# Kernel optimization log

Hardware: AMD Instinct MI355X
Metric: run time of the kernel (lower is better)

## Reference

```python
import jax, jax.numpy as jnp
import numpy as np

D = 1024
H = 16
DH = D // H


def setup_inputs() -> dict:
    key = jax.random.key(0)
    ks = jax.random.split(key, 9)
    s = 1.0 / np.sqrt(D)
    return {
        "x": jax.random.normal(ks[0], (4, 2048, D), dtype=jnp.float32),
        "wq": jax.random.uniform(ks[1], (D, D), jnp.float32, -s, s),
        "bq": jax.random.uniform(ks[2], (D,), jnp.float32, -s, s),
        "wk": jax.random.uniform(ks[3], (D, D), jnp.float32, -s, s),
        "bk": jax.random.uniform(ks[4], (D,), jnp.float32, -s, s),
        "wv": jax.random.uniform(ks[5], (D, D), jnp.float32, -s, s),
        "bv": jax.random.uniform(ks[6], (D,), jnp.float32, -s, s),
        "wo": jax.random.uniform(ks[7], (D, D), jnp.float32, -s, s),
        "bo": jax.random.uniform(ks[8], (D,), jnp.float32, -s, s),
    }


def reference(x, wq, bq, wk, bk, wv, bv, wo, bo):
    B, S, _ = x.shape
    # projections + split heads: [B, S, D] -> [B, H, S, Dh]
    def split(t):
        return t.reshape(B, S, H, DH).transpose(0, 2, 1, 3)
    q = split(x @ wq + bq)
    k = split(x @ wk + bk)
    v = split(x @ wv + bv)
    scale = 1.0 / jnp.sqrt(jnp.float32(DH))
    scores = jnp.einsum("bhqd,bhkd->bhqk", q, k) * scale  # [B,H,S,S]
    att = jax.nn.softmax(scores, axis=-1)
    out = jnp.einsum("bhqk,bhkd->bhqd", att, v)  # [B,H,S,Dh]
    out = out.transpose(0, 2, 1, 3).reshape(B, S, D)
    return out @ wo + bo
```

## Files before the change

### kernel.cpp

```cpp
#include <hip/hip_runtime.h>
#include <stdint.h>

typedef float f32x4 __attribute__((ext_vector_type(4)));
typedef __bf16 bf16x8 __attribute__((ext_vector_type(8)));
typedef unsigned short ushort_t;
typedef ushort_t ushortx8 __attribute__((ext_vector_type(8)));
typedef ushort_t ushortx4 __attribute__((ext_vector_type(4)));

#define DEV static __device__ __forceinline__

DEV ushort_t f2bf(float f) {
  union { float f; uint32_t u; } v; v.f = f;
  uint32_t u = v.u;
  return (ushort_t)((u + 0x7FFFu + ((u >> 16) & 1u)) >> 16);
}

DEV uint32_t pkbf(float a, float b) {
  __bf16 x = (__bf16)a, y = (__bf16)b;
  return (uint32_t)__builtin_bit_cast(unsigned short, x) |
         ((uint32_t)__builtin_bit_cast(unsigned short, y) << 16);
}

DEV void cp16(const void* g, void* l) {
  __builtin_amdgcn_global_load_lds((const __attribute__((address_space(1))) unsigned int*)g,
                                   (__attribute__((address_space(3))) unsigned int*)l,
                                   16, 0, 0);
}

DEV f32x4 mfma16(bf16x8 a, bf16x8 b, f32x4 c) {
  return __builtin_amdgcn_mfma_f32_16x16x32_bf16(a, b, c, 0, 0, 0);
}

__global__ __launch_bounds__(256) void k_prep(
    const float* __restrict__ x, ushort_t* __restrict__ xb,
    const float* __restrict__ wq, const float* __restrict__ wk,
    const float* __restrict__ wv, const float* __restrict__ wo,
    ushort_t* __restrict__ wqkvT, ushort_t* __restrict__ woT) {
  __shared__ float tile[32][33];
  int b = blockIdx.x;
  if (b < 4096) {
    size_t idx = ((size_t)b * 256 + threadIdx.x) * 8;
    const float4* src = (const float4*)(x + idx);
    float4 a = src[0], c = src[1];
    ushortx8 o;
    o[0] = f2bf(a.x); o[1] = f2bf(a.y); o[2] = f2bf(a.z); o[3] = f2bf(a.w);
    o[4] = f2bf(c.x); o[5] = f2bf(c.y); o[6] = f2bf(c.z); o[7] = f2bf(c.w);
    *(ushortx8*)(xb + idx) = o;
  } else {
    int t = b - 4096;
    int which = t >> 10;
    const float* src = (which == 0) ? wq : (which == 1) ? wk : (which == 2) ? wv : wo;
    ushort_t* dst = (which == 0) ? wqkvT
                    : (which == 1) ? wqkvT + 1024 * 1024
                    : (which == 2) ? wqkvT + 2 * 1024 * 1024
                                   : woT;
    int tt = t & 1023;
    int c0 = (tt & 31) * 32, r0 = (tt >> 5) * 32;
    int tx = threadIdx.x & 31, ty = threadIdx.x >> 5;
#pragma unroll
    for (int i = ty; i < 32; i += 8)
      tile[i][tx] = src[(size_t)(r0 + i) * 1024 + c0 + tx];
    __syncthreads();
#pragma unroll
    for (int i = ty; i < 32; i += 8)
      dst[(size_t)(c0 + i) * 1024 + r0 + tx] = f2bf(tile[tx][i]);
  }
}

__global__ __launch_bounds__(256) void k_transpose_v(const ushort_t* __restrict__ vw,
                                                     ushort_t* __restrict__ vtw) {
  __shared__ ushort_t t[64][72];
  int tid = threadIdx.x;
  int bh = blockIdx.y, s0 = blockIdx.x * 64;
#pragma unroll
  for (int n = 0; n < 2; ++n) {
    int row = (tid >> 3) + n * 32, ch = (tid & 7) * 8;
    *(ushortx8*)&t[row][ch] =
        *(const ushortx8*)&vw[((size_t)bh * 2048 + s0 + row) * 64 + ch];
  }
  __syncthreads();
#pragma unroll
  for (int n = 0; n < 2; ++n) {
    int dh = (tid >> 3) + n * 32, sc = (tid & 7) * 8;
    ushortx8 o;
#pragma unroll
    for (int k = 0; k < 8; ++k) o[k] = t[sc + k][dh];
    *(ushortx8*)&vtw[((size_t)bh * 64 + dh) * 2048 + s0 + sc] = o;
  }
}

template <int MODE>
__global__ __launch_bounds__(256, 2) void k_gemm(
    const ushort_t* __restrict__ A, const ushort_t* __restrict__ Bt,
    const float* __restrict__ b0, const float* __restrict__ b1,
    const float* __restrict__ b2, ushort_t* __restrict__ qw,
    ushort_t* __restrict__ kw, ushort_t* __restrict__ vw,
    float* __restrict__ outf) {
  const int K = 1024;
  __shared__ ushort_t As[128 * 32];
  __shared__ ushort_t Bs[128 * 32];
  int tid = threadIdx.x;
  int w = tid >> 6, lane = tid & 63, l16 = lane & 15, lg = lane >> 4;
  int m0 = blockIdx.x * 128, n0 = blockIdx.y * 128;
  int wm = (w >> 1) * 64, wn = (w & 1) * 64;
  f32x4 acc[4][4] = {};

  const ushort_t* Ag = A + (size_t)(m0 + (tid >> 2)) * K + (tid & 3) * 8;
  const ushort_t* Bg = Bt + (size_t)(n0 + (tid >> 2)) * K + (tid & 3) * 8;

  for (int k0 = 0; k0 < K; k0 += 32) {
    cp16(Ag + k0, As + w * 512);
    cp16(Ag + k0 + 64 * K, As + 2048 + w * 512);
    cp16(Bg + k0, Bs + w * 512);
    cp16(Bg + k0 + 64 * K, Bs + 2048 + w * 512);
    __syncthreads();
    bf16x8 af[4], bfr[4];
#pragma unroll
    for (int i = 0; i < 4; ++i)
      af[i] = *(const bf16x8*)&As[(wm + i * 16 + l16) * 32 + lg * 8];
#pragma unroll
    for (int j = 0; j < 4; ++j)
      bfr[j] = *(const bf16x8*)&Bs[(wn + j * 16 + l16) * 32 + lg * 8];
#pragma unroll
    for (int i = 0; i < 4; ++i)
#pragma unroll
      for (int j = 0; j < 4; ++j)
        acc[i][j] = mfma16(af[i], bfr[j], acc[i][j]);
    __syncthreads();
  }

  if (MODE == 0) {
    const float QSCALE = 0.18033688011112042f;
    int p = m0 >> 10;
    const float* bias = (p == 0) ? b0 : (p == 1) ? b1 : b2;
    ushort_t* dst = (p == 0) ? qw : (p == 1) ? kw : vw;
    float qs = (p == 0) ? QSCALE : 1.0f;
    int cbase = m0 & 1023;
#pragma unroll
    for (int i = 0; i < 4; ++i) {
      int oc = cbase + wm + i * 16 + lg * 4;
      int h = oc >> 6, dh0 = oc & 63;
      float4 bb = *(const float4*)&bias[oc];
#pragma unroll
      for (int j = 0; j < 4; ++j) {
        int tok = n0 + wn + j * 16 + l16;
        size_t base =
            ((size_t)((tok >> 11) * 16 + h) * 2048 + (tok & 2047)) * 64 + dh0;
        ushortx4 pk;
        pk[0] = f2bf((acc[i][j][0] + bb.x) * qs);
        pk[1] = f2bf((acc[i][j][1] + bb.y) * qs);
        pk[2] = f2bf((acc[i][j][2] + bb.z) * qs);
        pk[3] = f2bf((acc[i][j][3] + bb.w) * qs);
        *(ushortx4*)&dst[base] = pk;
      }
    }
  } else {
#pragma unroll
    for (int j = 0; j < 4; ++j) {
      int col = n0 + wn + j * 16 + l16;
      float bb = b0[col];
#pragma unroll
      for (int i = 0; i < 4; ++i) {
#pragma unroll
        for (int r = 0; r < 4; ++r) {
          int row = m0 + wm + i * 16 + lg * 4 + r;
          outf[(size_t)row * 1024 + col] = acc[i][j][r] + bb;
        }
      }
    }
  }
}

__global__ __launch_bounds__(512, 4) void k_attn(
    const ushort_t* __restrict__ qg, const ushort_t* __restrict__ kg,
    const ushort_t* __restrict__ vtg, ushort_t* __restrict__ att) {
  __shared__ ushort_t Ks[128 * 64];
  __shared__ ushort_t Vs[64 * 128];
  __shared__ ushort_t Ps[8][16 * 128];
  int tid = threadIdx.x;
  int w = tid >> 6, lane = tid & 63, l16 = lane & 15, lg = lane >> 4;
  int i = blockIdx.x;
  int bh = (i & 7) * 8 + ((i >> 3) & 7);
  int q0 = (i >> 6) * 256;
  const ushort_t* qh = qg + (size_t)bh * 2048 * 64;

  const ushort_t* kstage = kg + (size_t)bh * 2048 * 64 + (size_t)(tid >> 3) * 64 +
                           (size_t)(((tid & 7) ^ ((tid >> 3) & 7)) * 8);
  const ushort_t* vstage = vtg + (size_t)bh * 64 * 2048 + (size_t)(tid >> 4) * 2048 +
                           (size_t)(((tid & 15) ^ ((tid >> 4) & 15)) * 8);

  bf16x8 qf[2][2];
#pragma unroll
  for (int st = 0; st < 2; ++st)
#pragma unroll
    for (int ks = 0; ks < 2; ++ks)
      qf[st][ks] = *(const bf16x8*)(qh + (size_t)(q0 + w * 32 + st * 16 + l16) * 64 +
                                    ks * 32 + lg * 8);

  bf16x8 vone;
#pragma unroll
  for (int t = 0; t < 8; ++t) vone[t] = (__bf16)1.0f;

  f32x4 o[2][5] = {};

  for (int kb = 0; kb < 2048; kb += 128) {
    __syncthreads();
    cp16(kstage + (size_t)kb * 64, Ks + w * 512);
    cp16(kstage + (size_t)(kb + 64) * 64, Ks + 4096 + w * 512);
    cp16(vstage + kb, Vs + w * 512);
    cp16(vstage + kb + (size_t)32 * 2048, Vs + 4096 + w * 512);
    __syncthreads();

#pragma unroll
    for (int hf = 0; hf < 2; ++hf) {
      f32x4 sc[2][4] = {};
#pragma unroll
      for (int jt = 0; jt < 4; ++jt) {
        int row = hf * 64 + jt * 16 + l16;
        bf16x8 kf0 = *(const bf16x8*)&Ks[row * 64 + ((lg) ^ (l16 & 7)) * 8];
        bf16x8 kf1 = *(const bf16x8*)&Ks[row * 64 + ((lg + 4) ^ (l16 & 7)) * 8];
        sc[0][jt] = mfma16(kf0, qf[0][0], sc[0][jt]);
        sc[0][jt] = mfma16(kf1, qf[0][1], sc[0][jt]);
        sc[1][jt] = mfma16(kf0, qf[1][0], sc[1][jt]);
        sc[1][jt] = mfma16(kf1, qf[1][1], sc[1][jt]);
      }
#pragma unroll
      for (int st = 0; st < 2; ++st)
#pragma unroll
        for (int jt = 0; jt < 4; ++jt) {
          float e0 = __builtin_amdgcn_exp2f(sc[st][jt][0]);
          float e1 = __builtin_amdgcn_exp2f(sc[st][jt][1]);
          float e2 = __builtin_amdgcn_exp2f(sc[st][jt][2]);
          float e3 = __builtin_amdgcn_exp2f(sc[st][jt][3]);
          uint32_t* dst =
              (uint32_t*)&Ps[w][l16 * 128 +
                                (((st * 8 + jt * 2 + (lg >> 1)) ^ l16) * 8) +
                                (lg & 1) * 4];
          dst[0] = pkbf(e0, e1);
          dst[1] = pkbf(e2, e3);
        }
#pragma unroll
      for (int ks = 0; ks < 2; ++ks) {
        int kk = hf * 2 + ks;
        bf16x8 pf0 =
            *(const bf16x8*)&Ps[w][l16 * 128 + (((ks * 4 + lg) ^ l16) * 8)];
        bf16x8 pf1 =
            *(const bf16x8*)&Ps[w][l16 * 128 + (((8 + ks * 4 + lg) ^ l16) * 8)];
        o[0][4] = mfma16(pf0, vone, o[0][4]);
        o[1][4] = mfma16(pf1, vone, o[1][4]);
#pragma unroll
        for (int dt = 0; dt < 4; ++dt) {
          int vrow = dt * 16 + l16;
          bf16x8 vf =
              *(const bf16x8*)&Vs[vrow * 128 + (((kk * 4 + lg) ^ l16) * 8)];
          o[0][dt] = mfma16(pf0, vf, o[0][dt]);
          o[1][dt] = mfma16(pf1, vf, o[1][dt]);
        }
      }
    }
  }

  int bi = bh >> 4, h = bh & 15;
#pragma unroll
  for (int st = 0; st < 2; ++st) {
    f32x4 inv;
#pragma unroll
    for (int r = 0; r < 4; ++r) inv[r] = __builtin_amdgcn_rcpf(o[st][4][r]);
#pragma unroll
    for (int dt = 0; dt < 4; ++dt)
#pragma unroll
      for (int r = 0; r < 4; ++r) {
        int srow = q0 + w * 32 + st * 16 + lg * 4 + r;
        int col = h * 64 + dt * 16 + l16;
        att[(size_t)(bi * 2048 + srow) * 1024 + col] = f2bf(o[st][dt][r] * inv[r]);
      }
  }
}

extern "C" void kernel_launch(void* const* d_in, const int* in_sizes, int n_in,
                              void* d_out, int out_size, void* d_ws, size_t ws_size,
                              hipStream_t stream) {
  const float* x = (const float*)d_in[0];
  const float* wq = (const float*)d_in[1];
  const float* bq = (const float*)d_in[2];
  const float* wk = (const float*)d_in[3];
  const float* bk = (const float*)d_in[4];
  const float* wv = (const float*)d_in[5];
  const float* bv = (const float*)d_in[6];
  const float* wo = (const float*)d_in[7];
  const float* bo = (const float*)d_in[8];
  float* out = (float*)d_out;

  char* ws = (char*)d_ws;
  ushort_t* xb = (ushort_t*)(ws);
  ushort_t* wqkvT = (ushort_t*)(ws + 16777216);
  ushort_t* woT = (ushort_t*)(ws + 23068672);
  ushort_t* qw = (ushort_t*)(ws + 25165824);
  ushort_t* kw = (ushort_t*)(ws + 41943040);
  ushort_t* vtw = (ushort_t*)(ws + 58720256);
  ushort_t* att = (ushort_t*)(ws + 75497472);
  ushort_t* vw = att;

  k_prep<<<dim3(8192), dim3(256), 0, stream>>>(x, xb, wq, wk, wv, wo, wqkvT, woT);

  k_gemm<0><<<dim3(24, 64), dim3(256), 0, stream>>>(
      wqkvT, xb, bq, bk, bv, qw, kw, vw, nullptr);

  k_transpose_v<<<dim3(32, 64), dim3(256), 0, stream>>>(vw, vtw);

  k_attn<<<dim3(512), dim3(512), 0, stream>>>(qw, kw, vtw, att);

  k_gemm<1><<<dim3(64, 8), dim3(256), 0, stream>>>(
      att, woT, bo, nullptr, nullptr, nullptr, nullptr, nullptr, out);
}
```

Measured before the change: 277.2 us.

## Rewrite attention kernel with 32x32 MFMA tiles and register row sums

The attention kernel moves from 16x16x32 to 32x32x16 bf16 MFMA and halves the block to 4 waves, each handling 64 query rows. The softmax denominator is now summed in registers from the exp values and reduced across lane halves, which removes the extra ones-vector MFMA. The larger tiles are meant to raise the ratio of matrix math to LDS reads and cut LDS traffic per FLOP. In exchange each thread carries more accumulator registers and the occupancy target drops to 3 blocks per CU.

```diff
diff --git a/kernel.cpp b/kernel.cpp
--- a/kernel.cpp
+++ b/kernel.cpp
@@ -2,10 +2,12 @@
 #include <stdint.h>
 
 typedef float f32x4 __attribute__((ext_vector_type(4)));
+typedef float f32x16 __attribute__((ext_vector_type(16)));
 typedef __bf16 bf16x8 __attribute__((ext_vector_type(8)));
 typedef unsigned short ushort_t;
 typedef ushort_t ushortx8 __attribute__((ext_vector_type(8)));
 typedef ushort_t ushortx4 __attribute__((ext_vector_type(4)));
+typedef uint32_t u32x2 __attribute__((ext_vector_type(2)));
 
 #define DEV static __device__ __forceinline__
 
@@ -29,6 +31,10 @@
 
 DEV f32x4 mfma16(bf16x8 a, bf16x8 b, f32x4 c) {
   return __builtin_amdgcn_mfma_f32_16x16x32_bf16(a, b, c, 0, 0, 0);
+}
+
+DEV f32x16 mfma32(bf16x8 a, bf16x8 b, f32x16 c) {
+  return __builtin_amdgcn_mfma_f32_32x32x16_bf16(a, b, c, 0, 0, 0);
 }
 
 __global__ __launch_bounds__(256) void k_prep(
@@ -171,14 +177,14 @@
   }
 }
 
-__global__ __launch_bounds__(512, 4) void k_attn(
+__global__ __launch_bounds__(256, 3) void k_attn(
     const ushort_t* __restrict__ qg, const ushort_t* __restrict__ kg,
     const ushort_t* __restrict__ vtg, ushort_t* __restrict__ att) {
   __shared__ ushort_t Ks[128 * 64];
   __shared__ ushort_t Vs[64 * 128];
-  __shared__ ushort_t Ps[8][16 * 128];
+  __shared__ ushort_t Ps[4][2][32 * 32];
   int tid = threadIdx.x;
-  int w = tid >> 6, lane = tid & 63, l16 = lane & 15, lg = lane >> 4;
+  int w = tid >> 6, lane = tid & 63, l32 = lane & 31, half = lane >> 5;
   int i = blockIdx.x;
   int bh = (i & 7) * 8 + ((i >> 3) & 7);
   int q0 = (i >> 6) * 256;
@@ -189,90 +195,92 @@
   const ushort_t* vstage = vtg + (size_t)bh * 64 * 2048 + (size_t)(tid >> 4) * 2048 +
                            (size_t)(((tid & 15) ^ ((tid >> 4) & 15)) * 8);
 
-  bf16x8 qf[2][2];
+  bf16x8 qf[2][4];
 #pragma unroll
   for (int st = 0; st < 2; ++st)
 #pragma unroll
-    for (int ks = 0; ks < 2; ++ks)
-      qf[st][ks] = *(const bf16x8*)(qh + (size_t)(q0 + w * 32 + st * 16 + l16) * 64 +
-                                    ks * 32 + lg * 8);
-
-  bf16x8 vone;
-#pragma unroll
-  for (int t = 0; t < 8; ++t) vone[t] = (__bf16)1.0f;
-
-  f32x4 o[2][5] = {};
+    for (int ks = 0; ks < 4; ++ks)
+      qf[st][ks] = *(const bf16x8*)(qh +
+                                    (size_t)(q0 + w * 64 + st * 32 + l32) * 64 +
+                                    ks * 16 + half * 8);
+
+  f32x16 o[2][2] = {};
+  float lsum[2] = {0.f, 0.f};
+  int swz = (l32 >> 1) & 3;
 
   for (int kb = 0; kb < 2048; kb += 128) {
     __syncthreads();
-    cp16(kstage + (size_t)kb * 64, Ks + w * 512);
-    cp16(kstage + (size_t)(kb + 64) * 64, Ks + 4096 + w * 512);
-    cp16(vstage + kb, Vs + w * 512);
-    cp16(vstage + kb + (size_t)32 * 2048, Vs + 4096 + w * 512);
-    __syncthreads();
-
-#pragma unroll
-    for (int hf = 0; hf < 2; ++hf) {
-      f32x4 sc[2][4] = {};
-#pragma unroll
-      for (int jt = 0; jt < 4; ++jt) {
-        int row = hf * 64 + jt * 16 + l16;
-        bf16x8 kf0 = *(const bf16x8*)&Ks[row * 64 + ((lg) ^ (l16 & 7)) * 8];
-        bf16x8 kf1 = *(const bf16x8*)&Ks[row * 64 + ((lg + 4) ^ (l16 & 7)) * 8];
-        sc[0][jt] = mfma16(kf0, qf[0][0], sc[0][jt]);
-        sc[0][jt] = mfma16(kf1, qf[0][1], sc[0][jt]);
-        sc[1][jt] = mfma16(kf0, qf[1][0], sc[1][jt]);
-        sc[1][jt] = mfma16(kf1, qf[1][1], sc[1][jt]);
-      }
-#pragma unroll
-      for (int st = 0; st < 2; ++st)
-#pragma unroll
-        for (int jt = 0; jt < 4; ++jt) {
-          float e0 = __builtin_amdgcn_exp2f(sc[st][jt][0]);
-          float e1 = __builtin_amdgcn_exp2f(sc[st][jt][1]);
-          float e2 = __builtin_amdgcn_exp2f(sc[st][jt][2]);
-          float e3 = __builtin_amdgcn_exp2f(sc[st][jt][3]);
-          uint32_t* dst =
-              (uint32_t*)&Ps[w][l16 * 128 +
-                                (((st * 8 + jt * 2 + (lg >> 1)) ^ l16) * 8) +
-                                (lg & 1) * 4];
-          dst[0] = pkbf(e0, e1);
-          dst[1] = pkbf(e2, e3);
+#pragma unroll
+    for (int j = 0; j < 4; ++j) {
+      cp16(kstage + (size_t)(kb + j * 32) * 64, Ks + (j * 32 + w * 8) * 64);
+      cp16(vstage + kb + (size_t)(j * 16) * 2048, Vs + (j * 16 + w * 4) * 128);
+    }
+    __syncthreads();
+
+#pragma unroll
+    for (int g = 0; g < 4; ++g) {
+      bf16x8 kf[4];
+#pragma unroll
+      for (int ks = 0; ks < 4; ++ks)
+        kf[ks] = *(const bf16x8*)&Ks[(g * 32 + l32) * 64 +
+                                     (((2 * ks + half) ^ (l32 & 7)) * 8)];
+#pragma unroll
+      for (int st = 0; st < 2; ++st) {
+        f32x16 sc = {};
+#pragma unroll
+        for (int ks = 0; ks < 4; ++ks) sc = mfma32(kf[ks], qf[st][ks], sc);
+        float ls = 0.f;
+#pragma unroll
+        for (int r = 0; r < 16; ++r) {
+          sc[r] = __builtin_amdgcn_exp2f(sc[r]);
+          ls += sc[r];
         }
-#pragma unroll
-      for (int ks = 0; ks < 2; ++ks) {
-        int kk = hf * 2 + ks;
-        bf16x8 pf0 =
-            *(const bf16x8*)&Ps[w][l16 * 128 + (((ks * 4 + lg) ^ l16) * 8)];
-        bf16x8 pf1 =
-            *(const bf16x8*)&Ps[w][l16 * 128 + (((8 + ks * 4 + lg) ^ l16) * 8)];
-        o[0][4] = mfma16(pf0, vone, o[0][4]);
-        o[1][4] = mfma16(pf1, vone, o[1][4]);
-#pragma unroll
-        for (int dt = 0; dt < 4; ++dt) {
-          int vrow = dt * 16 + l16;
-          bf16x8 vf =
-              *(const bf16x8*)&Vs[vrow * 128 + (((kk * 4 + lg) ^ l16) * 8)];
-          o[0][dt] = mfma16(pf0, vf, o[0][dt]);
-          o[1][dt] = mfma16(pf1, vf, o[1][dt]);
+        lsum[st] += ls;
+#pragma unroll
+        for (int q2 = 0; q2 < 4; ++q2) {
+          u32x2 pk;
+          pk[0] = pkbf(sc[q2 * 4 + 0], sc[q2 * 4 + 1]);
+          pk[1] = pkbf(sc[q2 * 4 + 2], sc[q2 * 4 + 3]);
+          *(u32x2*)&Ps[w][st][l32 * 32 + ((q2 ^ swz) * 8) + half * 4] = pk;
         }
       }
+#pragma unroll
+      for (int ks2 = 0; ks2 < 2; ++ks2) {
+        int pofs = l32 * 32 + (((2 * ks2 + half) ^ swz) * 8);
+        bf16x8 pf0 = *(const bf16x8*)&Ps[w][0][pofs];
+        bf16x8 pf1 = *(const bf16x8*)&Ps[w][1][pofs];
+#pragma unroll
+        for (int dt = 0; dt < 2; ++dt) {
+          bf16x8 vf = *(const bf16x8*)&Vs[(dt * 32 + l32) * 128 +
+                                          (((4 * g + 2 * ks2 + half) ^
+                                            (l32 & 15)) * 8)];
+          o[0][dt] = mfma32(pf0, vf, o[0][dt]);
+          o[1][dt] = mfma32(pf1, vf, o[1][dt]);
+        }
+      }
     }
   }
 
+  float* lp = (float*)&Ps[w][0][0];
+#pragma unroll
+  for (int st = 0; st < 2; ++st) {
+    float lt = lsum[st] + __shfl_xor(lsum[st], 32);
+    if (half == 0) lp[st * 32 + l32] = __builtin_amdgcn_rcpf(lt);
+  }
   int bi = bh >> 4, h = bh & 15;
 #pragma unroll
   for (int st = 0; st < 2; ++st) {
-    f32x4 inv;
-#pragma unroll
-    for (int r = 0; r < 4; ++r) inv[r] = __builtin_amdgcn_rcpf(o[st][4][r]);
-#pragma unroll
-    for (int dt = 0; dt < 4; ++dt)
-#pragma unroll
-      for (int r = 0; r < 4; ++r) {
-        int srow = q0 + w * 32 + st * 16 + lg * 4 + r;
-        int col = h * 64 + dt * 16 + l16;
-        att[(size_t)(bi * 2048 + srow) * 1024 + col] = f2bf(o[st][dt][r] * inv[r]);
+    float linv[16];
+#pragma unroll
+    for (int r = 0; r < 16; ++r)
+      linv[r] = lp[st * 32 + ((r & 3) + 8 * (r >> 2) + 4 * half)];
+#pragma unroll
+    for (int dt = 0; dt < 2; ++dt)
+#pragma unroll
+      for (int r = 0; r < 16; ++r) {
+        int tok = q0 + w * 64 + st * 32 + (r & 3) + 8 * (r >> 2) + 4 * half;
+        att[(size_t)(bi * 2048 + tok) * 1024 + h * 64 + dt * 32 + l32] =
+            f2bf(o[st][dt][r] * linv[r]);
       }
   }
 }
@@ -308,7 +316,7 @@
 
   k_transpose_v<<<dim3(32, 64), dim3(256), 0, stream>>>(vw, vtw);
 
-  k_attn<<<dim3(512), dim3(512), 0, stream>>>(qw, kw, vtw, att);
+  k_attn<<<dim3(512), dim3(256), 0, stream>>>(qw, kw, vtw, att);
 
   k_gemm<1><<<dim3(64, 8), dim3(256), 0, stream>>>(
       att, woT, bo, nullptr, nullptr, nullptr, nullptr, nullptr, out);
```

Measured after the change: 616.3 us. 122% more time.
